# Optimization experiments

Hardware: AMD Instinct MI355X
Metric: run time of the kernel (lower is better)

Reference implementation:

```python
import jax, jax.numpy as jnp
import numpy as np

N, E, C, NE, G, T = 20000, 320000, 32, 10, 64, 1000
NB, HID, LAYERS = 8, 64, 2
R_MAX, P_CUT, AVG_NEIGH = 5.0, 6, 16.0
LM = 16  # (max_ell+1)^2 spherical-harmonic components
L_OF_LM = jnp.array([0,1,1,1,2,2,2,2,2,3,3,3,3,3,3,3])


def sph_harm(u):
    # component-normalized real spherical harmonics up to l=3 on unit vectors u [E,3]
    x, y, z = u[:, 0], u[:, 1], u[:, 2]
    s3, s15, s5, s105, s7 = 3**0.5, 15**0.5, 5**0.5, 105**0.5, 7**0.5
    s35_8, s21_8 = (35.0/8.0)**0.5, (21.0/8.0)**0.5
    comps = [jnp.ones_like(x),
             s3*x, s3*y, s3*z,
             s15*x*y, s15*y*z, 0.5*s5*(3*z*z-1.0), s15*x*z, 0.5*s15*(x*x-y*y),
             s35_8*y*(3*x*x-y*y), s105*x*y*z, s21_8*y*(5*z*z-1.0),
             0.5*s7*(5*z*z*z-3*z), s21_8*x*(5*z*z-1.0),
             0.5*s105*z*(x*x-y*y), s35_8*x*(x*x-3*y*y)]
    return jnp.stack(comps, axis=-1)  # [E,16]


def radial_embed(r):
    # Bessel basis with polynomial cutoff (MACE RadialEmbeddingBlock)
    n = jnp.arange(1, NB + 1, dtype=r.dtype)
    rc = jnp.maximum(r, 1e-9)
    bessel = (2.0/R_MAX)**0.5 * jnp.sin(n[None, :]*jnp.pi*rc[:, None]/R_MAX) / rc[:, None]
    xr = r / R_MAX
    p = float(P_CUT)
    f = (1.0 - 0.5*(p+1)*(p+2)*xr**p + p*(p+2)*xr**(p+1) - 0.5*p*(p+1)*xr**(p+2))
    f = f * (xr < 1.0)
    return bessel * f[:, None]  # [E,NB]


def setup_inputs():
    key = jax.random.key(0)
    ks = jax.random.split(key, 16)
    positions = jax.random.normal(ks[0], (N, 3)) * 3.0
    species = jax.random.randint(ks[1], (N,), 0, NE)
    node_attrs = jax.nn.one_hot(species, NE, dtype=jnp.float32)
    edge_index = jax.random.randint(ks[2], (2, E), 0, N)
    shifts = jnp.zeros((E, 3), jnp.float32)
    batch = jnp.sort(jax.random.randint(ks[3], (N,), 0, G))
    t = jax.random.randint(ks[4], (G,), 0, T)
    eps = jax.random.normal(ks[5], (N, NE + 3))
    betas = jnp.linspace(1e-4, 0.02, T)
    alpha_bar = jnp.cumprod(1.0 - betas)
    sc = 0.1
    W_embed = sc * jax.random.normal(ks[6], (NE + 1, C))
    W_r1 = sc * jax.random.normal(ks[7], (LAYERS, NB, HID))
    W_r2 = sc * jax.random.normal(ks[8], (LAYERS, HID, C * 4))
    W_mix = sc * jax.random.normal(ks[9], (LAYERS, 4, C, C))
    W_sc = sc * jax.random.normal(ks[10], (NE, C))
    W_prod = sc * jax.random.normal(ks[11], (LAYERS, 3, C))
    W_ro_s = sc * jax.random.normal(ks[12], (LAYERS, C, NE))
    W_ro_v = sc * jax.random.normal(ks[13], (LAYERS, C))
    return {"positions": positions, "node_attrs": node_attrs, "shifts": shifts,
            "eps": eps, "alpha_bar": alpha_bar, "W_embed": W_embed, "W_r1": W_r1,
            "W_r2": W_r2, "W_mix": W_mix, "W_sc": W_sc, "W_prod": W_prod,
            "W_ro_s": W_ro_s, "W_ro_v": W_ro_v, "edge_index": edge_index,
            "batch": batch, "t": t}


def reference(positions, node_attrs, shifts, eps, alpha_bar, W_embed, W_r1, W_r2,
              W_mix, W_sc, W_prod, W_ro_s, W_ro_v, edge_index, batch, t):
    sender, receiver = edge_index[0], edge_index[1]
    # diffusion: noise positions and attrs (DDPM q(x_t|x_0))
    ab = alpha_bar[t][batch][:, None]                       # [N,1]
    attrs0 = node_attrs / 4.0
    pos_noisy = jnp.sqrt(ab) * positions + jnp.sqrt(1.0 - ab) * eps[:, -3:]
    attrs_noisy = jnp.sqrt(ab) * attrs0 + jnp.sqrt(1.0 - ab) * eps[:, :NE]
    tf = (t.astype(jnp.float32) / T)[batch][:, None]
    h = jnp.concatenate([attrs_noisy, tf], axis=-1) @ W_embed  # [N,C]
    # edge geometry
    vec = pos_noisy[receiver] - pos_noisy[sender] + shifts
    r = jnp.sqrt(jnp.sum(vec * vec, axis=-1) + 1e-12)
    Y = sph_harm(vec / r[:, None])                          # [E,16]
    ef = radial_embed(r)                                    # [E,NB]
    scalar = h
    pred = jnp.zeros((N, NE + 3), h.dtype)
    for layer in range(LAYERS):
        rw = jax.nn.silu(ef @ W_r1[layer]) @ W_r2[layer]    # [E,4C]
        rw = rw.reshape(E, C, 4)[:, :, L_OF_LM]             # [E,C,16]
        msg = rw * scalar[sender][:, :, None] * Y[:, None, :]
        agg = jax.ops.segment_sum(msg, receiver, num_segments=N) / AVG_NEIGH
        Wm = W_mix[layer][L_OF_LM]                          # [16,C,C]
        feats = jnp.einsum('nck,kcd->ndk', agg, Wm)         # per-l channel mix
        s = feats[:, :, 0]
        poly = W_prod[layer, 0] + W_prod[layer, 1] * s + W_prod[layer, 2] * s * s
        feats = feats * poly[:, :, None]                    # correlation-3 product
        if layer == 0:
            feats = feats.at[:, :, 0].add(attrs_noisy @ W_sc)  # element skip
        scalar = feats[:, :, 0]
        pred_s = scalar @ W_ro_s[layer]                     # [N,NE]
        pred_v = jnp.einsum('ncm,c->nm', feats[:, :, 1:4], W_ro_v[layer])  # [N,3]
        pred = pred + jnp.concatenate([pred_s, pred_v], axis=-1)
    err = (pred - eps) ** 2
    loss_pos = jax.ops.segment_sum(err[:, -3:].sum(-1), batch, num_segments=G)
    loss_lab = jax.ops.segment_sum(err[:, :NE].sum(-1), batch, num_segments=G)
    nn = jax.ops.segment_sum(jnp.ones((N,), pred.dtype), batch, num_segments=G)
    loss = 0.5 * (loss_pos + loss_lab) / (jnp.maximum(nn, 1.0) * (3 + NE))
    return loss
```

## Files before the change

kernel.cpp:

```cpp
#include <hip/hip_runtime.h>

typedef unsigned short ushort_t;
typedef unsigned int uint_t;

#define NN 20000
#define EE 320000
#define CC 32
#define NEL 10
#define GG 64
#define TTT 1000
#define NBB 8
#define HIDD 64
#define EPB 128

typedef __attribute__((ext_vector_type(8))) short bf16x8;
typedef __attribute__((ext_vector_type(4))) float f32x4;

__device__ __forceinline__ float bits2f(uint_t b) { union { uint_t u; float f; } v; v.u = b; return v.f; }
__device__ __forceinline__ ushort_t f2b(float f) {
  union { float f; uint_t u; } v; v.f = f;
  uint_t r = (v.u + 0x7fffu + ((v.u >> 16) & 1u)) >> 16;
  return (ushort_t)r;
}
__device__ __forceinline__ uint_t pk(float a, float b) {
  return (uint_t)f2b(a) | ((uint_t)f2b(b) << 16);
}
__device__ __forceinline__ float lo16(uint_t u) { return bits2f(u << 16); }
__device__ __forceinline__ float hi16(uint_t u) { return bits2f(u & 0xffff0000u); }

__global__ __launch_bounds__(256) void k_prep(
    const float* __restrict__ positions, const float* __restrict__ node_attrs,
    const float* __restrict__ eps, const float* __restrict__ alpha_bar,
    const float* __restrict__ W_embed, const float* __restrict__ W_sc,
    const int* __restrict__ batch, const int* __restrict__ tarr,
    float* __restrict__ pos_noisy, float* __restrict__ scalA,
    float* __restrict__ sc_skip, float* __restrict__ pred, int* __restrict__ deg)
{
  int n = blockIdx.x * 256 + threadIdx.x;
  if (n >= NN) return;
  deg[n] = 0;
  int g = batch[n];
  int tn = tarr[g];
  float ab = alpha_bar[tn];
  float sa = sqrtf(ab), sb = sqrtf(fmaxf(1.0f - ab, 0.0f));
#pragma unroll
  for (int j = 0; j < 3; ++j)
    pos_noisy[n * 3 + j] = sa * positions[n * 3 + j] + sb * eps[n * 13 + 10 + j];
  float an[10];
#pragma unroll
  for (int j = 0; j < 10; ++j)
    an[j] = sa * 0.25f * node_attrs[n * 10 + j] + sb * eps[n * 13 + j];
  float tf = (float)tn * (1.0f / (float)TTT);
  for (int d = 0; d < CC; ++d) {
    float h = tf * W_embed[10 * CC + d];
    float sk = 0.0f;
#pragma unroll
    for (int j = 0; j < 10; ++j) {
      h = fmaf(an[j], W_embed[j * CC + d], h);
      sk = fmaf(an[j], W_sc[j * CC + d], sk);
    }
    scalA[n * CC + d] = h;
    sc_skip[n * CC + d] = sk;
  }
#pragma unroll
  for (int j = 0; j < 13; ++j) pred[n * 13 + j] = 0.0f;
}

__global__ __launch_bounds__(256) void k_edge_deg(const int* __restrict__ ei,
    int* __restrict__ deg)
{
  int e = blockIdx.x * 256 + threadIdx.x;
  atomicAdd(&deg[ei[EE + e]], 1);
}

__global__ __launch_bounds__(1024) void k_scan(const int* __restrict__ deg,
    int* __restrict__ offs, int* __restrict__ cursor,
    float* __restrict__ lnum, float* __restrict__ lcnt, int* __restrict__ ticket)
{
  __shared__ int wsums[16];
  __shared__ int woffs[16];
  int tid = threadIdx.x, lane = tid & 63, wv = tid >> 6;
  if (tid < GG) { lnum[tid] = 0.0f; lcnt[tid] = 0.0f; }
  if (tid == 64) *ticket = 0;
  int base = tid * 20;
  int loc[20];
  int s = 0;
#pragma unroll
  for (int j = 0; j < 20; ++j) {
    int idx = base + j;
    int v = (idx < NN) ? deg[idx] : 0;
    loc[j] = s; s += v;
  }
  int inc = s;
  for (int o = 1; o < 64; o <<= 1) {
    int v = __shfl_up(inc, o, 64);
    if (lane >= o) inc += v;
  }
  if (lane == 63) wsums[wv] = inc;
  __syncthreads();
  if (wv == 0 && lane < 16) {
    int v = wsums[lane];
    int i2 = v;
    for (int o = 1; o < 16; o <<= 1) {
      int vv = __shfl_up(i2, o, 16);
      if (lane >= o) i2 += vv;
    }
    woffs[lane] = i2 - v;
  }
  __syncthreads();
  int texcl = woffs[wv] + (inc - s);
#pragma unroll
  for (int j = 0; j < 20; ++j) {
    int idx = base + j;
    if (idx < NN) { int v = texcl + loc[j]; offs[idx] = v; cursor[idx] = v; }
  }
  if (tid == 1023) offs[NN] = EE;
}

__global__ __launch_bounds__(256) void k_edge2(
    const float* __restrict__ pos_noisy, const float* __restrict__ shifts,
    const int* __restrict__ ei, int* __restrict__ cursor,
    ushort_t* __restrict__ Ys, ushort_t* __restrict__ efs, int* __restrict__ snds)
{
  int e = blockIdx.x * 256 + threadIdx.x;
  int snd = ei[e], rcv = ei[EE + e];
  float vx = pos_noisy[rcv * 3 + 0] - pos_noisy[snd * 3 + 0] + shifts[e * 3 + 0];
  float vy = pos_noisy[rcv * 3 + 1] - pos_noisy[snd * 3 + 1] + shifts[e * 3 + 1];
  float vz = pos_noisy[rcv * 3 + 2] - pos_noisy[snd * 3 + 2] + shifts[e * 3 + 2];
  float r2 = vx * vx + vy * vy + vz * vz + 1e-12f;
  float r = sqrtf(r2);
  float inv = 1.0f / r;
  float x = vx * inv, y = vy * inv, z = vz * inv;

  const float s3 = 1.7320508075688772f, s15 = 3.872983346207417f, s5 = 2.23606797749979f;
  const float s105 = 10.246950765959598f, s7 = 2.6457513110645907f;
  const float s35_8 = 2.091650066335189f, s21_8 = 1.6201851746019651f;
  float yv[16];
  yv[0] = 1.0f;
  yv[1] = s3 * x; yv[2] = s3 * y; yv[3] = s3 * z;
  yv[4] = s15 * x * y;
  yv[5] = s15 * y * z;
  yv[6] = 0.5f * s5 * (3.0f * z * z - 1.0f);
  yv[7] = s15 * x * z;
  yv[8] = 0.5f * s15 * (x * x - y * y);
  yv[9] = s35_8 * y * (3.0f * x * x - y * y);
  yv[10] = s105 * x * y * z;
  yv[11] = s21_8 * y * (5.0f * z * z - 1.0f);
  yv[12] = 0.5f * s7 * (5.0f * z * z * z - 3.0f * z);
  yv[13] = s21_8 * x * (5.0f * z * z - 1.0f);
  yv[14] = 0.5f * s105 * z * (x * x - y * y);
  yv[15] = s35_8 * x * (x * x - 3.0f * y * y);

  float rc = fmaxf(r, 1e-9f);
  float pref = 0.6324555320336759f / rc;
  float th = 0.6283185307179586f * rc;
  float s1 = __sinf(th), c1 = __cosf(th);
  float xr = r * 0.2f;
  float fcut = 0.0f;
  if (xr < 1.0f) {
    float x2 = xr * xr, x3 = x2 * xr;
    float x6 = x3 * x3, x7 = x6 * xr, x8 = x7 * xr;
    fcut = 1.0f - 28.0f * x6 + 48.0f * x7 - 21.0f * x8;
  }
  float efv[8];
  float sp = 0.0f, scur = s1, c2 = 2.0f * c1;
#pragma unroll
  for (int b = 0; b < 8; ++b) {
    efv[b] = pref * scur * fcut;
    float nx = c2 * scur - sp;
    sp = scur; scur = nx;
  }

  int slot = atomicAdd(&cursor[rcv], 1);
  snds[slot] = snd;
  uint4* Y4 = (uint4*)Ys;
  Y4[(size_t)slot * 2 + 0] = make_uint4(pk(yv[0], yv[1]), pk(yv[2], yv[3]),
                                        pk(yv[4], yv[5]), pk(yv[6], yv[7]));
  Y4[(size_t)slot * 2 + 1] = make_uint4(pk(yv[8], yv[9]), pk(yv[10], yv[11]),
                                        pk(yv[12], yv[13]), pk(yv[14], yv[15]));
  ((uint4*)efs)[slot] = make_uint4(pk(efv[0], efv[1]), pk(efv[2], efv[3]),
                                   pk(efv[4], efv[5]), pk(efv[6], efv[7]));
}

__global__ __launch_bounds__(256) void k_rw2(
    const ushort_t* __restrict__ efs, const float* __restrict__ W_r1,
    const float* __restrict__ W_r2, const int* __restrict__ snds,
    const float* __restrict__ scal_in, ushort_t* __restrict__ rwc, int layer)
{
  __shared__ __align__(16) ushort_t w2t[128][72];
  __shared__ __align__(16) ushort_t h1t[EPB][72];
  __shared__ __align__(16) float w1s[NBB * HIDD];
  int tid = threadIdx.x;
  const float* W1g = W_r1 + layer * NBB * HIDD;
  const float* W2g = W_r2 + layer * HIDD * 128;
  for (int idx = tid; idx < HIDD * 128; idx += 256) {
    int k = idx >> 7, n = idx & 127;
    w2t[n][k] = f2b(W2g[idx]);
  }
  for (int i = tid; i < NBB * HIDD; i += 256) w1s[i] = W1g[i];
  __syncthreads();
  {
    int e = tid & 127, half = tid >> 7;
    uint4 q = ((const uint4*)efs)[(size_t)blockIdx.x * EPB + e];
    float ef8[8] = {lo16(q.x), hi16(q.x), lo16(q.y), hi16(q.y),
                    lo16(q.z), hi16(q.z), lo16(q.w), hi16(q.w)};
    for (int hc = 0; hc < 4; ++hc) {
      float v[8];
#pragma unroll
      for (int hh = 0; hh < 8; ++hh) {
        int h = half * 32 + hc * 8 + hh;
        float t = 0.0f;
#pragma unroll
        for (int b = 0; b < 8; ++b) t = fmaf(ef8[b], w1s[b * HIDD + h], t);
        v[hh] = t / (1.0f + __expf(-t));
      }
      *(uint4*)&h1t[e][half * 32 + hc * 8] =
          make_uint4(pk(v[0], v[1]), pk(v[2], v[3]), pk(v[4], v[5]), pk(v[6], v[7]));
    }
  }
  __syncthreads();
  int w = tid >> 6, lane = tid & 63;
  int c16 = lane & 15, quad = lane >> 4;
  bf16x8 afr[16];
#pragma unroll
  for (int nt = 0; nt < 8; ++nt) {
    afr[nt * 2 + 0] = *(const bf16x8*)&w2t[nt * 16 + c16][quad * 8];
    afr[nt * 2 + 1] = *(const bf16x8*)&w2t[nt * 16 + c16][32 + quad * 8];
  }
#pragma unroll
  for (int mt = 0; mt < 2; ++mt) {
    int mbase = w * 32 + mt * 16;
    bf16x8 b0 = *(const bf16x8*)&h1t[mbase + c16][quad * 8];
    bf16x8 b1 = *(const bf16x8*)&h1t[mbase + c16][32 + quad * 8];
    size_t eg = (size_t)blockIdx.x * EPB + mbase + c16;
    int snd = snds[eg];
    const float* sb = scal_in + (size_t)snd * CC + quad;
    float ssv[8];
#pragma unroll
    for (int nt = 0; nt < 8; ++nt) ssv[nt] = sb[nt * 4];
    uint2* dst = (uint2*)(rwc + eg * 128);
#pragma unroll
    for (int nt = 0; nt < 8; ++nt) {
      f32x4 acc = {0.0f, 0.0f, 0.0f, 0.0f};
      acc = __builtin_amdgcn_mfma_f32_16x16x32_bf16(afr[nt * 2 + 0], b0, acc, 0, 0, 0);
      acc = __builtin_amdgcn_mfma_f32_16x16x32_bf16(afr[nt * 2 + 1], b1, acc, 0, 0, 0);
      float s = ssv[nt];
      dst[nt * 4 + quad] = make_uint2(pk(acc[0] * s, acc[1] * s),
                                      pk(acc[2] * s, acc[3] * s));
    }
  }
}

__global__ __launch_bounds__(256) void k_layer(
    const ushort_t* __restrict__ Ys, const ushort_t* __restrict__ rwc,
    float* __restrict__ scal_out,
    const int* __restrict__ offs,
    const float* __restrict__ W_mix, const float* __restrict__ W_prod,
    const float* __restrict__ W_ro_s, const float* __restrict__ W_ro_v,
    const float* __restrict__ sc_skip, float* __restrict__ pred, int layer)
{
  __shared__ float lagg[4][CC][16];
  __shared__ float lf[4][CC][4];
  int w = threadIdx.x >> 6, lane = threadIdx.x & 63;
  int n = blockIdx.x * 4 + w;
  int c = lane >> 1;
  int kh = lane & 1;
  int kb = kh * 8;
  int i0 = offs[n], i1 = offs[n + 1];
  float acc0 = 0, acc1 = 0, acc2 = 0, acc3 = 0, acc4 = 0, acc5 = 0, acc6 = 0, acc7 = 0;
  const uint4* Y4 = (const uint4*)Ys;
  const uint2* rw2 = (const uint2*)rwc;
  int s = i0;
  for (; s + 4 <= i1; s += 4) {
    uint4 q0 = Y4[(size_t)(s + 0) * 2 + kh];
    uint2 p0 = rw2[(size_t)(s + 0) * 32 + c];
    uint4 q1 = Y4[(size_t)(s + 1) * 2 + kh];
    uint2 p1 = rw2[(size_t)(s + 1) * 32 + c];
    uint4 q2 = Y4[(size_t)(s + 2) * 2 + kh];
    uint2 p2 = rw2[(size_t)(s + 2) * 32 + c];
    uint4 q3 = Y4[(size_t)(s + 3) * 2 + kh];
    uint2 p3 = rw2[(size_t)(s + 3) * 32 + c];
#pragma unroll
    for (int u = 0; u < 4; ++u) {
      uint4 q = (u == 0) ? q0 : (u == 1) ? q1 : (u == 2) ? q2 : q3;
      uint2 rp = (u == 0) ? p0 : (u == 1) ? p1 : (u == 2) ? p2 : p3;
      float r0 = lo16(rp.x), r1 = hi16(rp.x), r2v = lo16(rp.y), r3 = hi16(rp.y);
      float w0 = kh ? r2v : r0, w13 = kh ? r3 : r1, w47 = kh ? r3 : r2v;
      acc0 = fmaf(w0,  lo16(q.x), acc0);
      acc1 = fmaf(w13, hi16(q.x), acc1);
      acc2 = fmaf(w13, lo16(q.y), acc2);
      acc3 = fmaf(w13, hi16(q.y), acc3);
      acc4 = fmaf(w47, lo16(q.z), acc4);
      acc5 = fmaf(w47, hi16(q.z), acc5);
      acc6 = fmaf(w47, lo16(q.w), acc6);
      acc7 = fmaf(w47, hi16(q.w), acc7);
    }
  }
  for (; s < i1; ++s) {
    uint4 q = Y4[(size_t)s * 2 + kh];
    uint2 rp = rw2[(size_t)s * 32 + c];
    float r0 = lo16(rp.x), r1 = hi16(rp.x), r2v = lo16(rp.y), r3 = hi16(rp.y);
    float w0 = kh ? r2v : r0, w13 = kh ? r3 : r1, w47 = kh ? r3 : r2v;
    acc0 = fmaf(w0,  lo16(q.x), acc0);
    acc1 = fmaf(w13, hi16(q.x), acc1);
    acc2 = fmaf(w13, lo16(q.y), acc2);
    acc3 = fmaf(w13, hi16(q.y), acc3);
    acc4 = fmaf(w47, lo16(q.z), acc4);
    acc5 = fmaf(w47, hi16(q.z), acc5);
    acc6 = fmaf(w47, lo16(q.w), acc6);
    acc7 = fmaf(w47, hi16(q.w), acc7);
  }
  const float invavg = 1.0f / 16.0f;
  lagg[w][c][kb + 0] = acc0 * invavg;
  lagg[w][c][kb + 1] = acc1 * invavg;
  lagg[w][c][kb + 2] = acc2 * invavg;
  lagg[w][c][kb + 3] = acc3 * invavg;
  lagg[w][c][kb + 4] = acc4 * invavg;
  lagg[w][c][kb + 5] = acc5 * invavg;
  lagg[w][c][kb + 6] = acc6 * invavg;
  lagg[w][c][kb + 7] = acc7 * invavg;
  __syncthreads();
  int d = c;
  float ft[8] = {0, 0, 0, 0, 0, 0, 0, 0};
  const float* Wm = W_mix + layer * 4096;
  for (int cc2 = 0; cc2 < CC; ++cc2) {
    float m0 = Wm[cc2 * CC + d];
    float m1 = Wm[1024 + cc2 * CC + d];
    float m2 = Wm[2048 + cc2 * CC + d];
    float m3 = Wm[3072 + cc2 * CC + d];
    float u0 = kh ? m2 : m0;
    float u13 = kh ? m3 : m1;
    float u47 = kh ? m3 : m2;
    ft[0] = fmaf(lagg[w][cc2][kb + 0], u0, ft[0]);
    ft[1] = fmaf(lagg[w][cc2][kb + 1], u13, ft[1]);
    ft[2] = fmaf(lagg[w][cc2][kb + 2], u13, ft[2]);
    ft[3] = fmaf(lagg[w][cc2][kb + 3], u13, ft[3]);
    ft[4] = fmaf(lagg[w][cc2][kb + 4], u47, ft[4]);
    ft[5] = fmaf(lagg[w][cc2][kb + 5], u47, ft[5]);
    ft[6] = fmaf(lagg[w][cc2][kb + 6], u47, ft[6]);
    ft[7] = fmaf(lagg[w][cc2][kb + 7], u47, ft[7]);
  }
  float sv = __shfl(ft[0], lane & 62, 64);
  const float* Wp = W_prod + layer * 96;
  float p0 = Wp[d], p1 = Wp[32 + d], p2 = Wp[64 + d];
  float poly = fmaf(fmaf(p2, sv, p1), sv, p0);
#pragma unroll
  for (int j = 0; j < 8; ++j) ft[j] *= poly;
  if (layer == 0 && kh == 0) ft[0] += sc_skip[n * CC + d];
  if (kh == 0) {
    scal_out[n * CC + d] = ft[0];
    lf[w][d][0] = ft[0]; lf[w][d][1] = ft[1]; lf[w][d][2] = ft[2]; lf[w][d][3] = ft[3];
  }
  __syncthreads();
  if (lane < 13) {
    float sum = 0.0f;
    if (lane < 10) {
      const float* Wr = W_ro_s + layer * CC * NEL;
      for (int dd = 0; dd < CC; ++dd) sum = fmaf(lf[w][dd][0], Wr[dd * NEL + lane], sum);
    } else {
      int mm = lane - 10;
      const float* Wv = W_ro_v + layer * CC;
      for (int dd = 0; dd < CC; ++dd) sum = fmaf(lf[w][dd][1 + mm], Wv[dd], sum);
    }
    pred[n * 13 + lane] += sum;
  }
}

__global__ __launch_bounds__(256) void k_loss(const float* __restrict__ pred,
    const float* __restrict__ eps, const int* __restrict__ batch,
    float* __restrict__ lnum, float* __restrict__ lcnt,
    int* __restrict__ ticket, float* __restrict__ out, int nblocks)
{
  __shared__ float psum[GG];
  __shared__ int pcnt[GG];
  __shared__ int lastflag;
  int tid = threadIdx.x;
  if (tid < GG) { psum[tid] = 0.0f; pcnt[tid] = 0; }
  __syncthreads();
  int n = blockIdx.x * 256 + tid;
  if (n < NN) {
    int g = batch[n];
    float sum = 0.0f;
#pragma unroll
    for (int j = 0; j < 13; ++j) {
      float dlt = pred[n * 13 + j] - eps[n * 13 + j];
      sum = fmaf(dlt, dlt, sum);
    }
    atomicAdd(&psum[g], sum);
    atomicAdd(&pcnt[g], 1);
  }
  __syncthreads();
  if (tid < GG && pcnt[tid] > 0) {
    atomicAdd(&lnum[tid], psum[tid]);
    atomicAdd(&lcnt[tid], (float)pcnt[tid]);
  }
  __syncthreads();
  if (tid == 0) {
    __threadfence();
    int t = atomicAdd(ticket, 1);
    lastflag = (t == nblocks - 1) ? 1 : 0;
  }
  __syncthreads();
  if (lastflag && tid < GG) {
    float num = atomicAdd(&lnum[tid], 0.0f);
    float cnt = atomicAdd(&lcnt[tid], 0.0f);
    out[tid] = 0.5f * num / (fmaxf(cnt, 1.0f) * 13.0f);
  }
}

extern "C" void kernel_launch(void* const* d_in, const int* in_sizes, int n_in,
                              void* d_out, int out_size, void* d_ws, size_t ws_size,
                              hipStream_t stream) {
  const float* positions  = (const float*)d_in[0];
  const float* node_attrs = (const float*)d_in[1];
  const float* shifts     = (const float*)d_in[2];
  const float* eps        = (const float*)d_in[3];
  const float* alpha_bar  = (const float*)d_in[4];
  const float* W_embed    = (const float*)d_in[5];
  const float* W_r1       = (const float*)d_in[6];
  const float* W_r2       = (const float*)d_in[7];
  const float* W_mix      = (const float*)d_in[8];
  const float* W_sc       = (const float*)d_in[9];
  const float* W_prod     = (const float*)d_in[10];
  const float* W_ro_s     = (const float*)d_in[11];
  const float* W_ro_v     = (const float*)d_in[12];
  const int* edge_index   = (const int*)d_in[13];
  const int* batch        = (const int*)d_in[14];
  const int* tarr         = (const int*)d_in[15];
  float* out = (float*)d_out;

  char* ws = (char*)d_ws;
  size_t off = 0;
  auto alloc = [&](size_t bytes) -> void* {
    void* p = ws + off;
    off = (off + bytes + 255) & ~(size_t)255;
    return p;
  };
  float* pos_noisy = (float*)alloc(NN * 3 * 4);
  float* scalA     = (float*)alloc(NN * CC * 4);
  float* scalB     = (float*)alloc(NN * CC * 4);
  float* sc_skip   = (float*)alloc(NN * CC * 4);
  float* pred      = (float*)alloc(NN * 13 * 4);
  ushort_t* Ys     = (ushort_t*)alloc((size_t)EE * 16 * 2);
  ushort_t* efs    = (ushort_t*)alloc((size_t)EE * 8 * 2);
  int* snds        = (int*)alloc((size_t)EE * 4);
  ushort_t* rwc    = (ushort_t*)alloc((size_t)EE * 128 * 2);
  int* deg         = (int*)alloc(NN * 4);
  int* offs        = (int*)alloc((NN + 1) * 4);
  int* cursor      = (int*)alloc(NN * 4);
  float* lnum      = (float*)alloc(GG * 4);
  float* lcnt      = (float*)alloc(GG * 4);
  int* ticket      = (int*)alloc(4);
  (void)ws_size; (void)in_sizes; (void)n_in; (void)out_size;

  const int NB_N = (NN + 255) / 256;
  const int NB_E = EE / 256;

  k_prep<<<NB_N, 256, 0, stream>>>(positions, node_attrs, eps, alpha_bar, W_embed,
                                   W_sc, batch, tarr, pos_noisy, scalA, sc_skip, pred, deg);
  k_edge_deg<<<NB_E, 256, 0, stream>>>(edge_index, deg);
  k_scan<<<1, 1024, 0, stream>>>(deg, offs, cursor, lnum, lcnt, ticket);
  k_edge2<<<NB_E, 256, 0, stream>>>(pos_noisy, shifts, edge_index, cursor, Ys, efs, snds);

  for (int layer = 0; layer < 2; ++layer) {
    const float* sin_p = (layer == 0) ? scalA : scalB;
    float* sout_p      = (layer == 0) ? scalB : scalA;
    k_rw2<<<EE / EPB, 256, 0, stream>>>(efs, W_r1, W_r2, snds, sin_p, rwc, layer);
    k_layer<<<NN / 4, 256, 0, stream>>>(Ys, rwc, sout_p, offs,
                                        W_mix, W_prod, W_ro_s, W_ro_v,
                                        sc_skip, pred, layer);
  }

  k_loss<<<NB_N, 256, 0, stream>>>(pred, eps, batch, lnum, lcnt, ticket, out, NB_N);
}
```

Before: 354.8 us.

## Fuse degree count with scan via last-block ticket and drop wave-local barriers

The edge-degree atomic kernel and the single-block scan kernel become one kernel. The last block to finish, detected by a global ticket, performs the prefix sum over node degrees, and the loss accumulators and tickets are now zeroed in the prep kernel. The aggregation loop in the layer kernel is unrolled by 2 instead of 4, and two __syncthreads are removed because each wave only reads its own shared-memory slice. This saves a kernel launch and block-wide barriers, but the fused scan runs on 256 threads, each doing 79 serial atomic reads twice, which may be slower than the old 1024-thread scan.

```diff
diff --git a/kernel.cpp b/kernel.cpp
--- a/kernel.cpp
+++ b/kernel.cpp
@@ -34,9 +34,12 @@
     const float* __restrict__ W_embed, const float* __restrict__ W_sc,
     const int* __restrict__ batch, const int* __restrict__ tarr,
     float* __restrict__ pos_noisy, float* __restrict__ scalA,
-    float* __restrict__ sc_skip, float* __restrict__ pred, int* __restrict__ deg)
+    float* __restrict__ sc_skip, float* __restrict__ pred, int* __restrict__ deg,
+    float* __restrict__ lnum, float* __restrict__ lcnt, int* __restrict__ tickets)
 {
   int n = blockIdx.x * 256 + threadIdx.x;
+  if (n == 0) { tickets[0] = 0; tickets[1] = 0; }
+  if (n < GG) { lnum[n] = 0.0f; lcnt[n] = 0.0f; }
   if (n >= NN) return;
   deg[n] = 0;
   int g = batch[n];
@@ -66,30 +69,30 @@
   for (int j = 0; j < 13; ++j) pred[n * 13 + j] = 0.0f;
 }
 
-__global__ __launch_bounds__(256) void k_edge_deg(const int* __restrict__ ei,
-    int* __restrict__ deg)
-{
-  int e = blockIdx.x * 256 + threadIdx.x;
+__global__ __launch_bounds__(256) void k_degscan(const int* __restrict__ ei,
+    int* __restrict__ deg, int* __restrict__ offs, int* __restrict__ cursor,
+    int* __restrict__ tickets)
+{
+  __shared__ int wsums[4];
+  __shared__ int lastflag;
+  int tid = threadIdx.x;
+  int e = blockIdx.x * 256 + tid;
   atomicAdd(&deg[ei[EE + e]], 1);
-}
-
-__global__ __launch_bounds__(1024) void k_scan(const int* __restrict__ deg,
-    int* __restrict__ offs, int* __restrict__ cursor,
-    float* __restrict__ lnum, float* __restrict__ lcnt, int* __restrict__ ticket)
-{
-  __shared__ int wsums[16];
-  __shared__ int woffs[16];
-  int tid = threadIdx.x, lane = tid & 63, wv = tid >> 6;
-  if (tid < GG) { lnum[tid] = 0.0f; lcnt[tid] = 0.0f; }
-  if (tid == 64) *ticket = 0;
-  int base = tid * 20;
-  int loc[20];
+  __syncthreads();
+  if (tid == 0) {
+    __threadfence();
+    int t = atomicAdd(&tickets[0], 1);
+    lastflag = (t == gridDim.x - 1) ? 1 : 0;
+  }
+  __syncthreads();
+  if (!lastflag) return;
+  int lane = tid & 63, wv = tid >> 6;
+  const int PER = (NN + 255) / 256;
+  int base = tid * PER;
   int s = 0;
-#pragma unroll
-  for (int j = 0; j < 20; ++j) {
+  for (int j = 0; j < PER; ++j) {
     int idx = base + j;
-    int v = (idx < NN) ? deg[idx] : 0;
-    loc[j] = s; s += v;
+    if (idx < NN) s += atomicAdd(&deg[idx], 0);
   }
   int inc = s;
   for (int o = 1; o < 64; o <<= 1) {
@@ -98,23 +101,22 @@
   }
   if (lane == 63) wsums[wv] = inc;
   __syncthreads();
-  if (wv == 0 && lane < 16) {
-    int v = wsums[lane];
-    int i2 = v;
-    for (int o = 1; o < 16; o <<= 1) {
-      int vv = __shfl_up(i2, o, 16);
-      if (lane >= o) i2 += vv;
-    }
-    woffs[lane] = i2 - v;
-  }
-  __syncthreads();
-  int texcl = woffs[wv] + (inc - s);
-#pragma unroll
-  for (int j = 0; j < 20; ++j) {
+  int woff = 0;
+  for (int i = 0; i < 4; ++i) {
+    int v = wsums[i];
+    if (i < wv) woff += v;
+  }
+  int excl = woff + (inc - s);
+  for (int j = 0; j < PER; ++j) {
     int idx = base + j;
-    if (idx < NN) { int v = texcl + loc[j]; offs[idx] = v; cursor[idx] = v; }
-  }
-  if (tid == 1023) offs[NN] = EE;
+    if (idx < NN) {
+      int v = atomicAdd(&deg[idx], 0);
+      offs[idx] = excl;
+      cursor[idx] = excl;
+      excl += v;
+    }
+  }
+  if (tid == 255) offs[NN] = EE;
 }
 
 __global__ __launch_bounds__(256) void k_edge2(
@@ -271,32 +273,37 @@
   const uint4* Y4 = (const uint4*)Ys;
   const uint2* rw2 = (const uint2*)rwc;
   int s = i0;
-  for (; s + 4 <= i1; s += 4) {
-    uint4 q0 = Y4[(size_t)(s + 0) * 2 + kh];
-    uint2 p0 = rw2[(size_t)(s + 0) * 32 + c];
-    uint4 q1 = Y4[(size_t)(s + 1) * 2 + kh];
-    uint2 p1 = rw2[(size_t)(s + 1) * 32 + c];
-    uint4 q2 = Y4[(size_t)(s + 2) * 2 + kh];
-    uint2 p2 = rw2[(size_t)(s + 2) * 32 + c];
-    uint4 q3 = Y4[(size_t)(s + 3) * 2 + kh];
-    uint2 p3 = rw2[(size_t)(s + 3) * 32 + c];
-#pragma unroll
-    for (int u = 0; u < 4; ++u) {
-      uint4 q = (u == 0) ? q0 : (u == 1) ? q1 : (u == 2) ? q2 : q3;
-      uint2 rp = (u == 0) ? p0 : (u == 1) ? p1 : (u == 2) ? p2 : p3;
-      float r0 = lo16(rp.x), r1 = hi16(rp.x), r2v = lo16(rp.y), r3 = hi16(rp.y);
+  for (; s + 2 <= i1; s += 2) {
+    uint4 qa = Y4[(size_t)s * 2 + kh];
+    uint2 ra = rw2[(size_t)s * 32 + c];
+    uint4 qb = Y4[(size_t)(s + 1) * 2 + kh];
+    uint2 rb = rw2[(size_t)(s + 1) * 32 + c];
+    {
+      float r0 = lo16(ra.x), r1 = hi16(ra.x), r2v = lo16(ra.y), r3 = hi16(ra.y);
       float w0 = kh ? r2v : r0, w13 = kh ? r3 : r1, w47 = kh ? r3 : r2v;
-      acc0 = fmaf(w0,  lo16(q.x), acc0);
-      acc1 = fmaf(w13, hi16(q.x), acc1);
-      acc2 = fmaf(w13, lo16(q.y), acc2);
-      acc3 = fmaf(w13, hi16(q.y), acc3);
-      acc4 = fmaf(w47, lo16(q.z), acc4);
-      acc5 = fmaf(w47, hi16(q.z), acc5);
-      acc6 = fmaf(w47, lo16(q.w), acc6);
-      acc7 = fmaf(w47, hi16(q.w), acc7);
-    }
-  }
-  for (; s < i1; ++s) {
+      acc0 = fmaf(w0,  lo16(qa.x), acc0);
+      acc1 = fmaf(w13, hi16(qa.x), acc1);
+      acc2 = fmaf(w13, lo16(qa.y), acc2);
+      acc3 = fmaf(w13, hi16(qa.y), acc3);
+      acc4 = fmaf(w47, lo16(qa.z), acc4);
+      acc5 = fmaf(w47, hi16(qa.z), acc5);
+      acc6 = fmaf(w47, lo16(qa.w), acc6);
+      acc7 = fmaf(w47, hi16(qa.w), acc7);
+    }
+    {
+      float r0 = lo16(rb.x), r1 = hi16(rb.x), r2v = lo16(rb.y), r3 = hi16(rb.y);
+      float w0 = kh ? r2v : r0, w13 = kh ? r3 : r1, w47 = kh ? r3 : r2v;
+      acc0 = fmaf(w0,  lo16(qb.x), acc0);
+      acc1 = fmaf(w13, hi16(qb.x), acc1);
+      acc2 = fmaf(w13, lo16(qb.y), acc2);
+      acc3 = fmaf(w13, hi16(qb.y), acc3);
+      acc4 = fmaf(w47, lo16(qb.z), acc4);
+      acc5 = fmaf(w47, hi16(qb.z), acc5);
+      acc6 = fmaf(w47, lo16(qb.w), acc6);
+      acc7 = fmaf(w47, hi16(qb.w), acc7);
+    }
+  }
+  if (s < i1) {
     uint4 q = Y4[(size_t)s * 2 + kh];
     uint2 rp = rw2[(size_t)s * 32 + c];
     float r0 = lo16(rp.x), r1 = hi16(rp.x), r2v = lo16(rp.y), r3 = hi16(rp.y);
@@ -319,7 +326,6 @@
   lagg[w][c][kb + 5] = acc5 * invavg;
   lagg[w][c][kb + 6] = acc6 * invavg;
   lagg[w][c][kb + 7] = acc7 * invavg;
-  __syncthreads();
   int d = c;
   float ft[8] = {0, 0, 0, 0, 0, 0, 0, 0};
   const float* Wm = W_mix + layer * 4096;
@@ -351,7 +357,6 @@
     scal_out[n * CC + d] = ft[0];
     lf[w][d][0] = ft[0]; lf[w][d][1] = ft[1]; lf[w][d][2] = ft[2]; lf[w][d][3] = ft[3];
   }
-  __syncthreads();
   if (lane < 13) {
     float sum = 0.0f;
     if (lane < 10) {
@@ -369,7 +374,7 @@
 __global__ __launch_bounds__(256) void k_loss(const float* __restrict__ pred,
     const float* __restrict__ eps, const int* __restrict__ batch,
     float* __restrict__ lnum, float* __restrict__ lcnt,
-    int* __restrict__ ticket, float* __restrict__ out, int nblocks)
+    int* __restrict__ tickets, float* __restrict__ out, int nblocks)
 {
   __shared__ float psum[GG];
   __shared__ int pcnt[GG];
@@ -397,7 +402,7 @@
   __syncthreads();
   if (tid == 0) {
     __threadfence();
-    int t = atomicAdd(ticket, 1);
+    int t = atomicAdd(&tickets[1], 1);
     lastflag = (t == nblocks - 1) ? 1 : 0;
   }
   __syncthreads();
@@ -450,16 +455,16 @@
   int* cursor      = (int*)alloc(NN * 4);
   float* lnum      = (float*)alloc(GG * 4);
   float* lcnt      = (float*)alloc(GG * 4);
-  int* ticket      = (int*)alloc(4);
+  int* tickets     = (int*)alloc(8);
   (void)ws_size; (void)in_sizes; (void)n_in; (void)out_size;
 
   const int NB_N = (NN + 255) / 256;
   const int NB_E = EE / 256;
 
   k_prep<<<NB_N, 256, 0, stream>>>(positions, node_attrs, eps, alpha_bar, W_embed,
-                                   W_sc, batch, tarr, pos_noisy, scalA, sc_skip, pred, deg);
-  k_edge_deg<<<NB_E, 256, 0, stream>>>(edge_index, deg);
-  k_scan<<<1, 1024, 0, stream>>>(deg, offs, cursor, lnum, lcnt, ticket);
+                                   W_sc, batch, tarr, pos_noisy, scalA, sc_skip,
+                                   pred, deg, lnum, lcnt, tickets);
+  k_degscan<<<NB_E, 256, 0, stream>>>(edge_index, deg, offs, cursor, tickets);
   k_edge2<<<NB_E, 256, 0, stream>>>(pos_noisy, shifts, edge_index, cursor, Ys, efs, snds);
 
   for (int layer = 0; layer < 2; ++layer) {
@@ -471,5 +476,5 @@
                                         sc_skip, pred, layer);
   }
 
-  k_loss<<<NB_N, 256, 0, stream>>>(pred, eps, batch, lnum, lcnt, ticket, out, NB_N);
-}
+  k_loss<<<NB_N, 256, 0, stream>>>(pred, eps, batch, lnum, lcnt, tickets, out, NB_N);
+}
```

Measured after the change: 396.1 us. 11.6% more time.
